# Kernel optimization log

Hardware: AMD Instinct MI355X
Metric: run time of the kernel (lower is better)

The kernel has to match this reference:

```python
import jax, jax.numpy as jnp
import numpy as np

N, F, U = 32768, 512, 512
GRID_SIZE, SPLINE_ORDER = 3, 3
GRID_RANGE = (-1.0, 1.0)
LN_EPS = 1e-3  # keras LayerNormalization default epsilon


def _make_grid():
    h = (GRID_RANGE[1] - GRID_RANGE[0]) / GRID_SIZE
    start = -SPLINE_ORDER * h + GRID_RANGE[0]
    stop = (GRID_SIZE + SPLINE_ORDER) * h + GRID_RANGE[0]
    num = GRID_SIZE + 2 * SPLINE_ORDER + 1  # 10 knots
    g = np.linspace(start, stop, num, dtype=np.float32)
    g = np.tile(g, (F, 1))[None, :, :]  # [1, F, num]
    return jnp.asarray(g)


def _glorot(key, shape):
    limit = np.sqrt(6.0 / (shape[0] + shape[1])).astype(np.float32)
    return jax.random.uniform(key, shape, jnp.float32, -limit, limit)


def setup_inputs() -> dict:
    key = jax.random.key(0)
    k_x, k_bw, k_sw = jax.random.split(key, 3)
    return {
        "x": jax.random.normal(k_x, (N, F), jnp.float32),
        "ln_gamma": jnp.ones((F,), jnp.float32),
        "ln_beta": jnp.zeros((F,), jnp.float32),
        "base_weight": _glorot(k_bw, (F, U)),
        "base_bias": jnp.zeros((U,), jnp.float32),
        "spline_weight": _glorot(k_sw, (F * (GRID_SIZE + SPLINE_ORDER), U)),
        "grid": _make_grid(),
    }


def _b_splines(x, grid):
    # x: [N, F]; grid: [1, F, G+2K+1]
    xe = x[..., None]  # [N, F, 1]
    bases = ((xe >= grid[..., :-1]) & (xe < grid[..., 1:])).astype(x.dtype)  # [N,F,G+2K]
    for k in range(1, SPLINE_ORDER + 1):
        left = (xe - grid[..., :-(k + 1)]) / (grid[..., k:-1] - grid[..., :-(k + 1)])
        right = (grid[..., k + 1:] - xe) / (grid[..., k + 1:] - grid[..., 1:-k])
        bases = left * bases[..., :-1] + right * bases[..., 1:]
    return bases.reshape(x.shape[0], -1)  # [N, F*(G+K)]


def reference(x, ln_gamma, ln_beta, base_weight, base_bias, spline_weight, grid):
    # LayerNorm over last axis
    mean = jnp.mean(x, axis=-1, keepdims=True)
    var = jnp.var(x, axis=-1, keepdims=True)
    xn = (x - mean) * jax.lax.rsqrt(var + LN_EPS) * ln_gamma + ln_beta
    # base branch: relu -> matmul -> bias
    base_out = jax.nn.relu(xn) @ base_weight + base_bias
    # spline branch: Cox-de Boor basis -> matmul
    spline_out = _b_splines(xn, grid) @ spline_weight
    # dropout rate 0 / inference -> identity
    return base_out + spline_out
```

## Files before the change

kernel.cpp:

```cpp
#include <hip/hip_runtime.h>
#include <hip/hip_bf16.h>


#define N_ROWS 32768
#define F_DIM  512
#define U_DIM  512
#define K_DIM  4096

typedef short short8 __attribute__((ext_vector_type(8)));
typedef float floatx4 __attribute__((ext_vector_type(4)));

__device__ __forceinline__ float bf2f(unsigned short h) {
    return __uint_as_float(((unsigned int)h) << 16);
}
__device__ __forceinline__ bool probe_bf16(const void* grid) {
    return ((const unsigned int*)grid)[0] != 0xC0400000u;
}
template <bool B16>
__device__ __forceinline__ float ldf(const void* p, int i) {
    return B16 ? bf2f(((const unsigned short*)p)[i]) : ((const float*)p)[i];
}
template <bool B16>
__device__ __forceinline__ void ld2(const void* p, int i, float* o) {
    if (B16) {
        ushort2 v = *(const ushort2*)((const unsigned short*)p + i);
        o[0] = bf2f(v.x); o[1] = bf2f(v.y);
    } else {
        float2 v = *(const float2*)((const float*)p + i);
        o[0] = v.x; o[1] = v.y;
    }
}
template <bool B16>
__device__ __forceinline__ void ld4(const void* p, int i, float* o) {
    if (B16) {
        ushort4 v = *(const ushort4*)((const unsigned short*)p + i);
        o[0] = bf2f(v.x); o[1] = bf2f(v.y); o[2] = bf2f(v.z); o[3] = bf2f(v.w);
    } else {
        float4 v = *(const float4*)((const float*)p + i);
        o[0] = v.x; o[1] = v.y; o[2] = v.z; o[3] = v.w;
    }
}
__device__ __forceinline__ unsigned int pk2(float lo, float hi) {
    __hip_bfloat162 h = __float22bfloat162_rn(make_float2(lo, hi));
    return *reinterpret_cast<unsigned int*>(&h);
}

template <bool B16>
__device__ __forceinline__ void ln_stats_body(const void* __restrict__ x,
                                              float2* __restrict__ stats) {
    int wave = threadIdx.x >> 6, lane = threadIdx.x & 63;
    int row = blockIdx.x * 4 + wave;
    float v[8];
    ld4<B16>(x, row * F_DIM + lane * 8, v);
    ld4<B16>(x, row * F_DIM + lane * 8 + 4, v + 4);
    float s = 0.f, s2 = 0.f;
#pragma unroll
    for (int k = 0; k < 8; ++k) { s += v[k]; s2 += v[k] * v[k]; }
#pragma unroll
    for (int off = 32; off > 0; off >>= 1) {
        s  += __shfl_xor(s, off);
        s2 += __shfl_xor(s2, off);
    }
    if (lane == 0) {
        float mean = s * (1.0f / F_DIM);
        float var  = s2 * (1.0f / F_DIM) - mean * mean;
        stats[row] = make_float2(mean, rsqrtf(var + 1e-3f));
    }
}
__global__ __launch_bounds__(256) void ln_stats_k(const void* __restrict__ x,
                                                  const void* __restrict__ grid,
                                                  float2* __restrict__ stats) {
    if (probe_bf16(grid)) ln_stats_body<true>(x, stats);
    else                  ln_stats_body<false>(x, stats);
}

template <bool B16>
__device__ __forceinline__ void build_wt_body(const void* __restrict__ bw,
                                              const void* __restrict__ sw,
                                              unsigned short* __restrict__ wt) {
    int idx = blockIdx.x * 256 + threadIdx.x;
    int u = idx & 511;
    int fq = idx >> 9;
#pragma unroll
    for (int i = 0; i < 4; ++i) {
        int f = fq * 4 + i;
        uint4 w;
        w.x = pk2(ldf<B16>(bw, f * U_DIM + u),            ldf<B16>(sw, (f * 6 + 0) * U_DIM + u));
        w.y = pk2(ldf<B16>(sw, (f * 6 + 1) * U_DIM + u),  ldf<B16>(sw, (f * 6 + 2) * U_DIM + u));
        w.z = pk2(ldf<B16>(sw, (f * 6 + 3) * U_DIM + u),  ldf<B16>(sw, (f * 6 + 4) * U_DIM + u));
        w.w = pk2(ldf<B16>(sw, (f * 6 + 5) * U_DIM + u),  0.f);
        *(uint4*)(wt + (size_t)u * K_DIM + f * 8) = w;
    }
}
__global__ __launch_bounds__(256) void build_wt_k(const void* __restrict__ bw,
                                                  const void* __restrict__ sw,
                                                  const void* __restrict__ grid,
                                                  unsigned short* __restrict__ wt) {
    if (probe_bf16(grid)) build_wt_body<true>(bw, sw, wt);
    else                  build_wt_body<false>(bw, sw, wt);
}

template <bool B16>
__device__ __forceinline__ void kan_gemm_body(
    const void* __restrict__ x,
    const float2* __restrict__ stats,
    const unsigned short* __restrict__ wt,
    const void* __restrict__ gam,
    const void* __restrict__ bet,
    const void* __restrict__ bias,
    void* __restrict__ out) {
    __shared__ __align__(16) unsigned short Alds[128 * 32];
    __shared__ __align__(16) unsigned short Blds[256 * 32];

    const int tid = threadIdx.x;
    const int lane = tid & 63, wv = tid >> 6;
    const int ctile = blockIdx.x;
    const int rtile = blockIdx.y;

    const int arow = tid & 127, fg = tid >> 7;
    const int grow = rtile * 128 + arow;
    float2 st = stats[grow];
    const float mean = st.x, rstd = st.y;
    const int xoff = grow * F_DIM + fg * 2;
    const int goff = fg * 2;
    const int aslot0 = ((arow >> 4) * 4 + fg * 2) * 16 + (arow & 15);
    uint4* aptr0 = (uint4*)&Alds[aslot0 * 8];
    uint4* aptr1 = (uint4*)&Alds[(aslot0 + 16) * 8];

    const unsigned short* gsrc[4];
    unsigned short* ldst[4];
#pragma unroll
    for (int i = 0; i < 4; ++i) {
        int s = wv * 256 + i * 64 + lane;
        int C = ((s >> 6) << 4) | (s & 15);
        int q = (s >> 4) & 3;
        gsrc[i] = wt + (size_t)(ctile * 256 + C) * K_DIM + q * 8;
        ldst[i] = &Blds[(wv * 256 + i * 64) * 8];
    }

    const int wr = wv >> 1, wc = wv & 1;
    const int lr = lane & 15, lq = lane >> 4;

    floatx4 acc[4][8];
#pragma unroll
    for (int mi = 0; mi < 4; ++mi)
#pragma unroll
        for (int ni = 0; ni < 8; ++ni) acc[mi][ni] = (floatx4){0.f, 0.f, 0.f, 0.f};

    for (int ks = 0; ks < K_DIM / 32; ++ks) {
#pragma unroll
        for (int i = 0; i < 4; ++i)
            __builtin_amdgcn_global_load_lds(
                (const __attribute__((address_space(1))) void*)(gsrc[i] + ks * 32),
                (__attribute__((address_space(3))) void*)ldst[i], 16, 0, 0);

        float xs[2], gs[2], bs[2];
        ld2<B16>(x, xoff + ks * 4, xs);
        ld2<B16>(gam, goff + ks * 4, gs);
        ld2<B16>(bet, goff + ks * 4, bs);
        uint4 pkv[2];
#pragma unroll
        for (int i = 0; i < 2; ++i) {
            float xn = fmaf(xs[i] - mean, rstd * gs[i], bs[i]);
            float tt = fmaf(xn, 1.5f, 4.5f);
            float bb[6];
#pragma unroll
            for (int j = 0; j < 6; ++j) {
                float d = tt - (float)(j + 2);
                float a = fabsf(d);
                float a2 = d * d;
                float v1 = fmaf(fmaf(0.5f, a, -1.0f), a2, 0.66666669f);
                float c = fmaxf(2.0f - a, 0.0f);
                float v2 = c * c * c * (1.0f / 6.0f);
                bb[j] = (a < 1.0f) ? v1 : v2;
            }
            pkv[i].x = pk2(fmaxf(xn, 0.f), bb[0]);
            pkv[i].y = pk2(bb[1], bb[2]);
            pkv[i].z = pk2(bb[3], bb[4]);
            pkv[i].w = pk2(bb[5], 0.f);
        }
        *aptr0 = pkv[0];
        *aptr1 = pkv[1];
        __syncthreads();

        short8 afr[4], bfr[8];
#pragma unroll
        for (int mi = 0; mi < 4; ++mi)
            afr[mi] = *(const short8*)&Alds[((wr * 4 + mi) * 64 + lane) * 8];
#pragma unroll
        for (int ni = 0; ni < 8; ++ni)
            bfr[ni] = *(const short8*)&Blds[((wc * 8 + ni) * 64 + lane) * 8];
#pragma unroll
        for (int mi = 0; mi < 4; ++mi)
#pragma unroll
            for (int ni = 0; ni < 8; ++ni)
                acc[mi][ni] = __builtin_amdgcn_mfma_f32_16x16x32_bf16(
                    afr[mi], bfr[ni], acc[mi][ni], 0, 0, 0);
        __syncthreads();
    }

    float biasv[8];
#pragma unroll
    for (int ni = 0; ni < 8; ++ni)
        biasv[ni] = ldf<B16>(bias, ctile * 256 + wc * 128 + ni * 16 + lr);
#pragma unroll
    for (int mi = 0; mi < 4; ++mi)
#pragma unroll
        for (int ni = 0; ni < 8; ++ni)
#pragma unroll
            for (int r = 0; r < 4; ++r) {
                int row = rtile * 128 + wr * 64 + mi * 16 + lq * 4 + r;
                int col = ctile * 256 + wc * 128 + ni * 16 + lr;
                float val = acc[mi][ni][r] + biasv[ni];
                if (B16) ((unsigned short*)out)[(size_t)row * U_DIM + col] =
                    (unsigned short)(pk2(val, 0.f) & 0xffffu);
                else ((float*)out)[(size_t)row * U_DIM + col] = val;
            }
}
__global__ __launch_bounds__(256, 2) void kan_gemm(
    const void* __restrict__ x, const float2* __restrict__ stats,
    const unsigned short* __restrict__ wt, const void* __restrict__ gam,
    const void* __restrict__ bet, const void* __restrict__ bias,
    const void* __restrict__ grid, void* __restrict__ out) {
    if (probe_bf16(grid)) kan_gemm_body<true>(x, stats, wt, gam, bet, bias, out);
    else                  kan_gemm_body<false>(x, stats, wt, gam, bet, bias, out);
}

extern "C" void kernel_launch(void* const* d_in, const int* in_sizes, int n_in,
                              void* d_out, int out_size, void* d_ws, size_t ws_size,
                              hipStream_t stream) {
    const void* x    = d_in[0];
    const void* gam  = d_in[1];
    const void* bet  = d_in[2];
    const void* bw   = d_in[3];
    const void* bb   = d_in[4];
    const void* sw   = d_in[5];
    const void* grid = d_in[6];

    float2* stats = (float2*)d_ws;
    unsigned short* wt = (unsigned short*)((char*)d_ws + N_ROWS * sizeof(float2));

    hipLaunchKernelGGL(ln_stats_k, dim3(N_ROWS / 4), dim3(256), 0, stream, x, grid, stats);
    hipLaunchKernelGGL(build_wt_k, dim3(U_DIM * 128 / 256), dim3(256), 0, stream,
                       bw, sw, grid, wt);
    hipLaunchKernelGGL(kan_gemm, dim3(2, N_ROWS / 128), dim3(256), 0, stream,
                       x, stats, wt, gam, bet, bb, grid, d_out);
}
```

Measured before the change: 310.9 us.

## Double-buffer GEMM K-loop, widen tile to full U, merge prep kernels

The GEMM now uses 512-thread blocks covering all 512 output columns per 128-row tile, so the spline basis for each row is generated once instead of twice. LDS buffers for A and B are double-buffered: the next B slice is prefetched with global_load_lds and the next A basis chunk is computed while MFMAs run on the current one, leaving one barrier per iteration. The LN-stats and weight-pack kernels are fused into a single launch. The trade-offs are a grid of only 256 blocks, double the LDS use, and register pressure under launch bounds of 512 threads with 2 blocks per CU.

```diff
diff --git a/kernel.cpp b/kernel.cpp
--- a/kernel.cpp
+++ b/kernel.cpp
@@ -19,16 +19,6 @@
 template <bool B16>
 __device__ __forceinline__ float ldf(const void* p, int i) {
     return B16 ? bf2f(((const unsigned short*)p)[i]) : ((const float*)p)[i];
-}
-template <bool B16>
-__device__ __forceinline__ void ld2(const void* p, int i, float* o) {
-    if (B16) {
-        ushort2 v = *(const ushort2*)((const unsigned short*)p + i);
-        o[0] = bf2f(v.x); o[1] = bf2f(v.y);
-    } else {
-        float2 v = *(const float2*)((const float*)p + i);
-        o[0] = v.x; o[1] = v.y;
-    }
 }
 template <bool B16>
 __device__ __forceinline__ void ld4(const void* p, int i, float* o) {
@@ -47,9 +37,9 @@
 
 template <bool B16>
 __device__ __forceinline__ void ln_stats_body(const void* __restrict__ x,
-                                              float2* __restrict__ stats) {
+                                              float2* __restrict__ stats, int bid) {
     int wave = threadIdx.x >> 6, lane = threadIdx.x & 63;
-    int row = blockIdx.x * 4 + wave;
+    int row = bid * 4 + wave;
     float v[8];
     ld4<B16>(x, row * F_DIM + lane * 8, v);
     ld4<B16>(x, row * F_DIM + lane * 8 + 4, v + 4);
@@ -67,18 +57,11 @@
         stats[row] = make_float2(mean, rsqrtf(var + 1e-3f));
     }
 }
-__global__ __launch_bounds__(256) void ln_stats_k(const void* __restrict__ x,
-                                                  const void* __restrict__ grid,
-                                                  float2* __restrict__ stats) {
-    if (probe_bf16(grid)) ln_stats_body<true>(x, stats);
-    else                  ln_stats_body<false>(x, stats);
-}
-
 template <bool B16>
 __device__ __forceinline__ void build_wt_body(const void* __restrict__ bw,
                                               const void* __restrict__ sw,
-                                              unsigned short* __restrict__ wt) {
-    int idx = blockIdx.x * 256 + threadIdx.x;
+                                              unsigned short* __restrict__ wt, int bid) {
+    int idx = bid * 256 + threadIdx.x;
     int u = idx & 511;
     int fq = idx >> 9;
 #pragma unroll
@@ -92,12 +75,49 @@
         *(uint4*)(wt + (size_t)u * K_DIM + f * 8) = w;
     }
 }
-__global__ __launch_bounds__(256) void build_wt_k(const void* __restrict__ bw,
-                                                  const void* __restrict__ sw,
-                                                  const void* __restrict__ grid,
-                                                  unsigned short* __restrict__ wt) {
-    if (probe_bf16(grid)) build_wt_body<true>(bw, sw, wt);
-    else                  build_wt_body<false>(bw, sw, wt);
+__global__ __launch_bounds__(256) void prep_k(const void* __restrict__ x,
+                                              const void* __restrict__ bw,
+                                              const void* __restrict__ sw,
+                                              const void* __restrict__ grid,
+                                              float2* __restrict__ stats,
+                                              unsigned short* __restrict__ wt) {
+    int bid = blockIdx.x;
+    if (probe_bf16(grid)) {
+        if (bid < N_ROWS / 4) ln_stats_body<true>(x, stats, bid);
+        else                  build_wt_body<true>(bw, sw, wt, bid - N_ROWS / 4);
+    } else {
+        if (bid < N_ROWS / 4) ln_stats_body<false>(x, stats, bid);
+        else                  build_wt_body<false>(bw, sw, wt, bid - N_ROWS / 4);
+    }
+}
+
+template <bool B16>
+__device__ __forceinline__ uint4 gen_a_pack(const void* __restrict__ x,
+                                            const void* __restrict__ gam,
+                                            const void* __restrict__ bet,
+                                            int xrow, int f, float mean, float rstd) {
+    float xv = ldf<B16>(x, xrow + f);
+    float gv = ldf<B16>(gam, f);
+    float bv = ldf<B16>(bet, f);
+    float xn = fmaf(xv - mean, rstd * gv, bv);
+    float tt = fmaf(xn, 1.5f, 4.5f);
+    float bb[6];
+#pragma unroll
+    for (int j = 0; j < 6; ++j) {
+        float d = tt - (float)(j + 2);
+        float a = fabsf(d);
+        float a2 = d * d;
+        float v1 = fmaf(fmaf(0.5f, a, -1.0f), a2, 0.66666669f);
+        float c = fmaxf(2.0f - a, 0.0f);
+        float v2 = c * c * c * (1.0f / 6.0f);
+        bb[j] = (a < 1.0f) ? v1 : v2;
+    }
+    uint4 o;
+    o.x = pk2(fmaxf(xn, 0.f), bb[0]);
+    o.y = pk2(bb[1], bb[2]);
+    o.z = pk2(bb[3], bb[4]);
+    o.w = pk2(bb[5], 0.f);
+    return o;
 }
 
 template <bool B16>
@@ -109,36 +129,31 @@
     const void* __restrict__ bet,
     const void* __restrict__ bias,
     void* __restrict__ out) {
-    __shared__ __align__(16) unsigned short Alds[128 * 32];
-    __shared__ __align__(16) unsigned short Blds[256 * 32];
+    __shared__ __align__(16) unsigned short Alds[2][128 * 32];
+    __shared__ __align__(16) unsigned short Blds[2][2048 * 8];
 
     const int tid = threadIdx.x;
     const int lane = tid & 63, wv = tid >> 6;
-    const int ctile = blockIdx.x;
-    const int rtile = blockIdx.y;
+    const int rtile = blockIdx.x;
 
     const int arow = tid & 127, fg = tid >> 7;
     const int grow = rtile * 128 + arow;
-    float2 st = stats[grow];
+    const float2 st = stats[grow];
     const float mean = st.x, rstd = st.y;
-    const int xoff = grow * F_DIM + fg * 2;
-    const int goff = fg * 2;
-    const int aslot0 = ((arow >> 4) * 4 + fg * 2) * 16 + (arow & 15);
-    uint4* aptr0 = (uint4*)&Alds[aslot0 * 8];
-    uint4* aptr1 = (uint4*)&Alds[(aslot0 + 16) * 8];
+    const int xrow = grow * F_DIM;
+    const int aslot = ((arow >> 4) * 4 + fg) * 16 + (arow & 15);
 
     const unsigned short* gsrc[4];
-    unsigned short* ldst[4];
 #pragma unroll
     for (int i = 0; i < 4; ++i) {
         int s = wv * 256 + i * 64 + lane;
         int C = ((s >> 6) << 4) | (s & 15);
         int q = (s >> 4) & 3;
-        gsrc[i] = wt + (size_t)(ctile * 256 + C) * K_DIM + q * 8;
-        ldst[i] = &Blds[(wv * 256 + i * 64) * 8];
-    }
-
-    const int wr = wv >> 1, wc = wv & 1;
+        gsrc[i] = wt + (size_t)C * K_DIM + q * 8;
+    }
+    const int bbase = (wv * 256) * 8;
+
+    const int wr = wv >> 2, wc = wv & 3;
     const int lr = lane & 15, lq = lane >> 4;
 
     floatx4 acc[4][8];
@@ -147,62 +162,67 @@
 #pragma unroll
         for (int ni = 0; ni < 8; ++ni) acc[mi][ni] = (floatx4){0.f, 0.f, 0.f, 0.f};
 
-    for (int ks = 0; ks < K_DIM / 32; ++ks) {
+#pragma unroll
+    for (int i = 0; i < 4; ++i)
+        __builtin_amdgcn_global_load_lds(
+            (const __attribute__((address_space(1))) void*)gsrc[i],
+            (__attribute__((address_space(3))) void*)&Blds[0][bbase + i * 64 * 8], 16, 0, 0);
+    {
+        uint4 p0 = gen_a_pack<B16>(x, gam, bet, xrow, fg, mean, rstd);
+        *(uint4*)&Alds[0][aslot * 8] = p0;
+    }
+    __syncthreads();
+
+    for (int ks = 0; ks < K_DIM / 32 - 1; ++ks) {
+        const int cur = ks & 1, nxt = cur ^ 1;
+
 #pragma unroll
         for (int i = 0; i < 4; ++i)
             __builtin_amdgcn_global_load_lds(
-                (const __attribute__((address_space(1))) void*)(gsrc[i] + ks * 32),
-                (__attribute__((address_space(3))) void*)ldst[i], 16, 0, 0);
-
-        float xs[2], gs[2], bs[2];
-        ld2<B16>(x, xoff + ks * 4, xs);
-        ld2<B16>(gam, goff + ks * 4, gs);
-        ld2<B16>(bet, goff + ks * 4, bs);
-        uint4 pkv[2];
-#pragma unroll
-        for (int i = 0; i < 2; ++i) {
-            float xn = fmaf(xs[i] - mean, rstd * gs[i], bs[i]);
-            float tt = fmaf(xn, 1.5f, 4.5f);
-            float bb[6];
-#pragma unroll
-            for (int j = 0; j < 6; ++j) {
-                float d = tt - (float)(j + 2);
-                float a = fabsf(d);
-                float a2 = d * d;
-                float v1 = fmaf(fmaf(0.5f, a, -1.0f), a2, 0.66666669f);
-                float c = fmaxf(2.0f - a, 0.0f);
-                float v2 = c * c * c * (1.0f / 6.0f);
-                bb[j] = (a < 1.0f) ? v1 : v2;
-            }
-            pkv[i].x = pk2(fmaxf(xn, 0.f), bb[0]);
-            pkv[i].y = pk2(bb[1], bb[2]);
-            pkv[i].z = pk2(bb[3], bb[4]);
-            pkv[i].w = pk2(bb[5], 0.f);
-        }
-        *aptr0 = pkv[0];
-        *aptr1 = pkv[1];
-        __syncthreads();
+                (const __attribute__((address_space(1))) void*)(gsrc[i] + (ks + 1) * 32),
+                (__attribute__((address_space(3))) void*)&Blds[nxt][bbase + i * 64 * 8], 16, 0, 0);
 
         short8 afr[4], bfr[8];
 #pragma unroll
         for (int mi = 0; mi < 4; ++mi)
-            afr[mi] = *(const short8*)&Alds[((wr * 4 + mi) * 64 + lane) * 8];
+            afr[mi] = *(const short8*)&Alds[cur][((wr * 4 + mi) * 64 + lane) * 8];
 #pragma unroll
         for (int ni = 0; ni < 8; ++ni)
-            bfr[ni] = *(const short8*)&Blds[((wc * 8 + ni) * 64 + lane) * 8];
+            bfr[ni] = *(const short8*)&Blds[cur][((wc * 8 + ni) * 64 + lane) * 8];
+
+        uint4 pkv = gen_a_pack<B16>(x, gam, bet, xrow, (ks + 1) * 4 + fg, mean, rstd);
+        *(uint4*)&Alds[nxt][aslot * 8] = pkv;
+
 #pragma unroll
         for (int mi = 0; mi < 4; ++mi)
 #pragma unroll
             for (int ni = 0; ni < 8; ++ni)
                 acc[mi][ni] = __builtin_amdgcn_mfma_f32_16x16x32_bf16(
                     afr[mi], bfr[ni], acc[mi][ni], 0, 0, 0);
+
         __syncthreads();
     }
 
+    {
+        short8 afr[4], bfr[8];
+#pragma unroll
+        for (int mi = 0; mi < 4; ++mi)
+            afr[mi] = *(const short8*)&Alds[1][((wr * 4 + mi) * 64 + lane) * 8];
+#pragma unroll
+        for (int ni = 0; ni < 8; ++ni)
+            bfr[ni] = *(const short8*)&Blds[1][((wc * 8 + ni) * 64 + lane) * 8];
+#pragma unroll
+        for (int mi = 0; mi < 4; ++mi)
+#pragma unroll
+            for (int ni = 0; ni < 8; ++ni)
+                acc[mi][ni] = __builtin_amdgcn_mfma_f32_16x16x32_bf16(
+                    afr[mi], bfr[ni], acc[mi][ni], 0, 0, 0);
+    }
+
     float biasv[8];
 #pragma unroll
     for (int ni = 0; ni < 8; ++ni)
-        biasv[ni] = ldf<B16>(bias, ctile * 256 + wc * 128 + ni * 16 + lr);
+        biasv[ni] = ldf<B16>(bias, wc * 128 + ni * 16 + lr);
 #pragma unroll
     for (int mi = 0; mi < 4; ++mi)
 #pragma unroll
@@ -210,14 +230,14 @@
 #pragma unroll
             for (int r = 0; r < 4; ++r) {
                 int row = rtile * 128 + wr * 64 + mi * 16 + lq * 4 + r;
-                int col = ctile * 256 + wc * 128 + ni * 16 + lr;
+                int col = wc * 128 + ni * 16 + lr;
                 float val = acc[mi][ni][r] + biasv[ni];
                 if (B16) ((unsigned short*)out)[(size_t)row * U_DIM + col] =
                     (unsigned short)(pk2(val, 0.f) & 0xffffu);
                 else ((float*)out)[(size_t)row * U_DIM + col] = val;
             }
 }
-__global__ __launch_bounds__(256, 2) void kan_gemm(
+__global__ __launch_bounds__(512, 2) void kan_gemm(
     const void* __restrict__ x, const float2* __restrict__ stats,
     const unsigned short* __restrict__ wt, const void* __restrict__ gam,
     const void* __restrict__ bet, const void* __restrict__ bias,
@@ -240,9 +260,8 @@
     float2* stats = (float2*)d_ws;
     unsigned short* wt = (unsigned short*)((char*)d_ws + N_ROWS * sizeof(float2));
 
-    hipLaunchKernelGGL(ln_stats_k, dim3(N_ROWS / 4), dim3(256), 0, stream, x, grid, stats);
-    hipLaunchKernelGGL(build_wt_k, dim3(U_DIM * 128 / 256), dim3(256), 0, stream,
-                       bw, sw, grid, wt);
-    hipLaunchKernelGGL(kan_gemm, dim3(2, N_ROWS / 128), dim3(256), 0, stream,
+    hipLaunchKernelGGL(prep_k, dim3(N_ROWS / 4 + U_DIM * 128 / 256), dim3(256), 0, stream,
+                       x, bw, sw, grid, stats, wt);
+    hipLaunchKernelGGL(kan_gemm, dim3(N_ROWS / 128), dim3(512), 0, stream,
                        x, stats, wt, gam, bet, bb, grid, d_out);
 }
```

Result: slower. 356.2 us (+14.6%).
